# Performance work log

Measured on AMD Instinct MI355X. Metric: run time of the kernel, lower is better.

The kernel has to match this reference:

```python
import jax, jax.numpy as jnp
import numpy as np

N = 100000       # nodes
E = 1600000      # edges (avg degree 16)
F_IN = 128
F_OUT = 128
EPS = 1e-5       # GraphNorm eps
NEG_SLOPE = 0.01 # nn.LeakyReLU default


def setup_inputs() -> dict:
    key = jax.random.key(0)
    ks = jax.random.split(key, 4)
    x = jax.random.normal(ks[0], (N, F_IN), dtype=jnp.float32)
    edge_index = jax.random.randint(ks[1], (2, E), 0, N, dtype=jnp.int64)
    # GCNConv linear weight (stored as [in, out] for x @ W)
    W = jax.random.normal(ks[2], (F_IN, F_OUT), dtype=jnp.float32) / np.sqrt(F_IN).astype(np.float32)
    b = jnp.zeros((F_OUT,), jnp.float32)          # GCNConv bias
    gn_weight = jnp.ones((F_OUT,), jnp.float32)   # GraphNorm weight
    gn_bias = jnp.zeros((F_OUT,), jnp.float32)    # GraphNorm bias
    gn_mean_scale = jnp.ones((F_OUT,), jnp.float32)  # GraphNorm mean_scale
    return {"x": x, "edge_index": edge_index, "W": W, "b": b,
            "gn_weight": gn_weight, "gn_bias": gn_bias, "gn_mean_scale": gn_mean_scale}


def reference(x, edge_index, W, b, gn_weight, gn_bias, gn_mean_scale):
    n = x.shape[0]
    # --- GCNConv with add_self_loops=True, symmetric normalization ---
    loops = jnp.arange(n, dtype=edge_index.dtype)
    src = jnp.concatenate([edge_index[0], loops])  # [E+N]
    dst = jnp.concatenate([edge_index[1], loops])  # [E+N]
    deg = jax.ops.segment_sum(jnp.ones(src.shape, x.dtype), dst, num_segments=n)  # [N]
    deg_inv_sqrt = jnp.where(deg > 0, 1.0 / jnp.sqrt(deg), 0.0)
    norm = deg_inv_sqrt[src] * deg_inv_sqrt[dst]   # [E+N]
    h = x @ W                                      # [N, F_OUT]
    agg = jax.ops.segment_sum(h[src] * norm[:, None], dst, num_segments=n) + b  # [N, F_OUT]
    # --- GraphNorm (single graph: stats over all nodes, per-feature) ---
    mean = jnp.mean(agg, axis=0)                   # [F_OUT]
    centered = agg - mean * gn_mean_scale
    var = jnp.mean(centered * centered, axis=0)
    out = centered / jnp.sqrt(var + EPS) * gn_weight + gn_bias
    # --- LeakyReLU ---
    out = jnp.where(out > 0, out, NEG_SLOPE * out)
    return (out, edge_index)
```

## Files before the change

kernel.cpp:

```cpp
#include <hip/hip_runtime.h>

#define NN 100000
#define NE 1600000
#define F  128
#define NSPL 50000

#define SH   8
#define NPB  256
#define NBKT 391
#define B1   256
#define CH1  6250
#define MATN (NBKT * B1)
#define MATP (98 * 1024)
#define BCAP2 6144

#define SB   256

constexpr float EPS   = 1e-5f;
constexpr float SLOPE = 0.01f;

typedef __attribute__((ext_vector_type(8))) short short8;
typedef __attribute__((ext_vector_type(4))) float f32x4;
typedef __attribute__((ext_vector_type(2))) float f32x2;

__device__ inline unsigned int bf16rne(float f) {
    unsigned int u = __float_as_uint(f);
    return (u + 0x7fffu + ((u >> 16) & 1u)) >> 16;
}
__device__ inline float blo(unsigned int u) { return __uint_as_float(u << 16); }
__device__ inline float bhi(unsigned int u) { return __uint_as_float(u & 0xffff0000u); }
__device__ inline unsigned int pack2(float a, float b) {
    return bf16rne(a) | (bf16rne(b) << 16);
}
__device__ inline f32x2 pkadd(f32x2 a, f32x2 b) {
    f32x2 d;
    asm("v_pk_add_f32 %0, %1, %2" : "=v"(d) : "v"(a), "v"(b));
    return d;
}
__device__ inline f32x2 up2n(unsigned int u) {
    f32x2 r;
    r.x = __uint_as_float(u << 16);
    r.y = __uint_as_float(u);
    return r;
}

__global__ void k_wprep(const float* __restrict__ Wm, unsigned int* __restrict__ Wt) {
    int idx = blockIdx.x * 256 + threadIdx.x;
    int p = idx & 3, lane = (idx >> 2) & 63, n = (idx >> 8) & 7, kk = idx >> 11;
    int k0 = kk * 32 + (lane >> 4) * 8 + 2 * p;
    int c  = n * 16 + (lane & 15);
    unsigned int lo = bf16rne(Wm[k0 * F + c]);
    unsigned int hi = bf16rne(Wm[(k0 + 1) * F + c]);
    Wt[idx] = lo | (hi << 16);
}

__global__ __launch_bounds__(1024) void k_hist1(const int* __restrict__ dst,
                                                unsigned int* __restrict__ mat) {
    __shared__ unsigned int h[NBKT];
    if (threadIdx.x < NBKT) h[threadIdx.x] = 0u;
    __syncthreads();
    const int e0 = blockIdx.x * CH1;
    for (int i = threadIdx.x; i < CH1; i += 1024)
        atomicAdd(&h[dst[e0 + i] >> SH], 1u);
    __syncthreads();
    if (threadIdx.x < NBKT) mat[threadIdx.x * B1 + blockIdx.x] = h[threadIdx.x];
}

__global__ __launch_bounds__(1024) void k_scanA(const unsigned int* __restrict__ mat,
                                                unsigned int* __restrict__ scn,
                                                unsigned int* __restrict__ bsums) {
    __shared__ unsigned int ps[1024];
    const int t = threadIdx.x;
    const int i = blockIdx.x * 1024 + t;
    unsigned int v = mat[i];
    ps[t] = v;
    __syncthreads();
    for (int off = 1; off < 1024; off <<= 1) {
        unsigned int a = (t >= off) ? ps[t - off] : 0u;
        __syncthreads();
        ps[t] += a;
        __syncthreads();
    }
    scn[i] = ps[t];
    if (t == 1023) bsums[blockIdx.x] = ps[1023];
}

__global__ __launch_bounds__(128) void k_scanB(const unsigned int* __restrict__ bsums,
                                               unsigned int* __restrict__ boff) {
    __shared__ unsigned int ps[128];
    const int t = threadIdx.x;
    unsigned int v = (t < 98) ? bsums[t] : 0u;
    ps[t] = v;
    __syncthreads();
    for (int off = 1; off < 128; off <<= 1) {
        unsigned int a = (t >= off) ? ps[t - off] : 0u;
        __syncthreads();
        ps[t] += a;
        __syncthreads();
    }
    if (t < 98) boff[t] = ps[t] - v;
}


__global__ __launch_bounds__(1024) void k_scat1(const int* __restrict__ ei,
                                                const unsigned int* __restrict__ mat,
                                                const unsigned int* __restrict__ scn,
                                                const unsigned int* __restrict__ boff,
                                                unsigned int* __restrict__ ebuf) {
    __shared__ unsigned int cur[NBKT];
    if (threadIdx.x < NBKT) {
        int idx = threadIdx.x * B1 + blockIdx.x;
        cur[threadIdx.x] = scn[idx] + boff[idx >> 10] - mat[idx];
    }
    __syncthreads();
    const int e0 = blockIdx.x * CH1;
    for (int i = threadIdx.x; i < CH1; i += 1024) {
        int s = ei[e0 + i];
        int d = ei[NE + e0 + i];
        unsigned int pos = atomicAdd(&cur[d >> SH], 1u);
        ebuf[pos] = ((unsigned int)(d & (NPB - 1)) << 17) | (unsigned int)s;
    }
}

__global__ __launch_bounds__(256) void k_fill2(const unsigned int* __restrict__ mat,
                                               const unsigned int* __restrict__ scn,
                                               const unsigned int* __restrict__ boff,
                                               const unsigned int* __restrict__ ebuf,
                                               int* __restrict__ row_start,
                                               float* __restrict__ dis,
                                               int* __restrict__ csr) {
    __shared__ unsigned int stage[BCAP2];
    __shared__ unsigned int hist[NPB];
    __shared__ unsigned int cur[NPB];
    __shared__ unsigned int ps[NPB];
    const int t = threadIdx.x;
    const int bkt = blockIdx.x;
    hist[t] = 0u;
    __syncthreads();
    const int i0 = bkt * B1;
    const unsigned int ebase = scn[i0] + boff[i0 >> 10] - mat[i0];
    unsigned int eend;
    if (bkt == NBKT - 1) eend = (unsigned int)NE;
    else {
        const int i1 = (bkt + 1) * B1;
        eend = scn[i1] + boff[i1 >> 10] - mat[i1];
    }
    const unsigned int n = eend - ebase;
    const unsigned int m = (n < BCAP2) ? n : BCAP2;
    for (unsigned int i = t; i < m; i += 256) {
        unsigned int v = ebuf[ebase + i];
        stage[i] = v;
        atomicAdd(&hist[v >> 17], 1u);
    }
    for (unsigned int i = BCAP2 + t; i < n; i += 256)
        atomicAdd(&hist[ebuf[ebase + i] >> 17], 1u);
    __syncthreads();
    const unsigned int deg = hist[t];
    ps[t] = deg;
    __syncthreads();
    for (int off = 1; off < 256; off <<= 1) {
        unsigned int a = (t >= off) ? ps[t - off] : 0u;
        __syncthreads();
        ps[t] += a;
        __syncthreads();
    }
    const unsigned int ex = (t == 0) ? 0u : ps[t - 1];
    cur[t] = ebase + ex;
    const int node = bkt * NPB + t;
    if (node <= NN) row_start[node] = (int)(ebase + ex);
    if (node < NN)  dis[node] = rsqrtf((float)(deg + 1u));
    __syncthreads();
    for (unsigned int i = t; i < m; i += 256) {
        unsigned int v = stage[i];
        unsigned int pos = atomicAdd(&cur[v >> 17], 1u);
        csr[pos] = (int)(v & 0x1FFFFu);
    }
    for (unsigned int i = BCAP2 + t; i < n; i += 256) {
        unsigned int v = ebuf[ebase + i];
        unsigned int pos = atomicAdd(&cur[v >> 17], 1u);
        csr[pos] = (int)(v & 0x1FFFFu);
    }
}

__global__ __launch_bounds__(256) void k_gemm(const float* __restrict__ x,
                                              const unsigned int* __restrict__ Wt,
                                              const float* __restrict__ dis,
                                              unsigned short* __restrict__ g16) {
    __shared__ unsigned int xl[128 * 64];
    const int tid = threadIdx.x;
    const int lane = tid & 63, wave = tid >> 6;
    const int row0 = blockIdx.x * 128;

#pragma unroll
    for (int i = 0; i < 16; ++i) {
        int fi = i * 256 + tid;
        int lr = fi >> 5;
        int cf = (fi & 31) * 4;
        int gr = row0 + lr; if (gr >= NN) gr = NN - 1;
        float4 v = *(const float4*)(x + (size_t)gr * F + cf);
        unsigned int u0 = pack2(v.x, v.y);
        unsigned int u1 = pack2(v.z, v.w);
        int cu = (cf >> 1) ^ ((lr & 7) << 2);
        uint2 w2; w2.x = u0; w2.y = u1;
        *(uint2*)&xl[lr * 64 + cu] = w2;
    }
    __syncthreads();

    const int rbase = row0 + wave * 32;
    short8 afr[2][4];
#pragma unroll
    for (int m = 0; m < 2; ++m) {
        int lr = wave * 32 + m * 16 + (lane & 15);
#pragma unroll
        for (int kk = 0; kk < 4; ++kk) {
            int cu = (kk * 16 + (lane >> 4) * 4) ^ ((lr & 7) << 2);
            afr[m][kk] = *(const short8*)&xl[lr * 64 + cu];
        }
    }

    f32x4 acc[2][8];
#pragma unroll
    for (int m = 0; m < 2; ++m)
#pragma unroll
        for (int n = 0; n < 8; ++n) { f32x4 z = {0.f, 0.f, 0.f, 0.f}; acc[m][n] = z; }

    const uint4* Wt4 = (const uint4*)Wt;
#pragma unroll
    for (int kk = 0; kk < 4; ++kk) {
        union { uint4 u; short8 s; } bfr[8];
#pragma unroll
        for (int n = 0; n < 8; ++n) bfr[n].u = Wt4[(kk * 8 + n) * 64 + lane];
#pragma unroll
        for (int m = 0; m < 2; ++m)
#pragma unroll
            for (int n = 0; n < 8; ++n)
                acc[m][n] = __builtin_amdgcn_mfma_f32_16x16x32_bf16(afr[m][kk], bfr[n].s, acc[m][n], 0, 0, 0);
    }

    float dv[2][4];
#pragma unroll
    for (int m = 0; m < 2; ++m)
#pragma unroll
        for (int r = 0; r < 4; ++r) {
            int row = rbase + m * 16 + (lane >> 4) * 4 + r;
            dv[m][r] = (row < NN) ? dis[row] : 0.0f;
        }
#pragma unroll
    for (int m = 0; m < 2; ++m)
#pragma unroll
        for (int n = 0; n < 8; ++n)
#pragma unroll
            for (int r = 0; r < 4; ++r) {
                int row = rbase + m * 16 + (lane >> 4) * 4 + r;
                if (row < NN) {
                    int col = n * 16 + (lane & 15);
                    g16[(size_t)row * F + col] = (unsigned short)bf16rne(acc[m][n][r] * dv[m][r]);
                }
            }
}

__global__ __launch_bounds__(256) void k_gather(const unsigned int* __restrict__ g,
                                                const int* __restrict__ csr,
                                                const int* __restrict__ row_start,
                                                const float* __restrict__ dis,
                                                const float* __restrict__ b,
                                                unsigned int* __restrict__ agg_lo,
                                                unsigned int* __restrict__ agg_hi) {
    const int lane = threadIdx.x & 63;
    const int node = blockIdx.x * 4 + (threadIdx.x >> 6);
    if (node >= NN) return;
    const int q = lane >> 4;
    const int c = lane & 15;
    const int j = row_start[node];
    const int e = row_start[node + 1];
    const int L = e - j + 1;
    int sv = (j + lane < e) ? csr[j + lane] : node;
    f32x2 A0 = {0.f, 0.f}, A1 = A0, A2 = A0, A3 = A0;
    int k = 0;
    const int L1 = (L < 64) ? L : 64;
    for (; k < L1; k += 16) {
        int k0 = k + q, k1 = k0 + 4, k2 = k0 + 8, k3 = k0 + 12;
        int r0 = __shfl(sv, k0);
        int r1 = __shfl(sv, k1);
        int r2 = __shfl(sv, k2);
        int r3 = __shfl(sv, k3);
        bool p0 = k0 < L, p1 = k1 < L, p2 = k2 < L, p3 = k3 < L;
        uint4 v0, v1, v2, v3;
        if (p0) v0 = *(const uint4*)&g[(size_t)r0 * 64 + c * 4];
        if (p1) v1 = *(const uint4*)&g[(size_t)r1 * 64 + c * 4];
        if (p2) v2 = *(const uint4*)&g[(size_t)r2 * 64 + c * 4];
        if (p3) v3 = *(const uint4*)&g[(size_t)r3 * 64 + c * 4];
        if (p0) {
            A0 = pkadd(A0, up2n(v0.x)); A1 = pkadd(A1, up2n(v0.y));
            A2 = pkadd(A2, up2n(v0.z)); A3 = pkadd(A3, up2n(v0.w));
        }
        if (p1) {
            A0 = pkadd(A0, up2n(v1.x)); A1 = pkadd(A1, up2n(v1.y));
            A2 = pkadd(A2, up2n(v1.z)); A3 = pkadd(A3, up2n(v1.w));
        }
        if (p2) {
            A0 = pkadd(A0, up2n(v2.x)); A1 = pkadd(A1, up2n(v2.y));
            A2 = pkadd(A2, up2n(v2.z)); A3 = pkadd(A3, up2n(v2.w));
        }
        if (p3) {
            A0 = pkadd(A0, up2n(v3.x)); A1 = pkadd(A1, up2n(v3.y));
            A2 = pkadd(A2, up2n(v3.z)); A3 = pkadd(A3, up2n(v3.w));
        }
    }
    for (; k < L; k += 16) {
#pragma unroll
        for (int s = 0; s < 4; ++s) {
            int ks = k + q + s * 4;
            if (ks < L) {
                int rs = (j + ks < e) ? csr[j + ks] : node;
                uint4 v = *(const uint4*)&g[(size_t)rs * 64 + c * 4];
                A0 = pkadd(A0, up2n(v.x)); A1 = pkadd(A1, up2n(v.y));
                A2 = pkadd(A2, up2n(v.z)); A3 = pkadd(A3, up2n(v.w));
            }
        }
    }
#define RED2(A) A.x += __shfl_xor(A.x, 16); A.x += __shfl_xor(A.x, 32); \
                A.y += __shfl_xor(A.y, 16); A.y += __shfl_xor(A.y, 32);
    RED2(A0) RED2(A1) RED2(A2) RED2(A3)
#undef RED2
    if (q == 0) {
        float d = dis[node];
        const float4* bp = (const float4*)&b[c * 8];
        float4 b0 = bp[0], b1 = bp[1];
        uint4 w;
        w.x = pack2(b0.x + d * A0.x, b0.y + d * A0.y);
        w.y = pack2(b0.z + d * A1.x, b0.w + d * A1.y);
        w.z = pack2(b1.x + d * A2.x, b1.y + d * A2.y);
        w.w = pack2(b1.z + d * A3.x, b1.w + d * A3.y);
        unsigned int* base = (node < NSPL) ? (agg_lo + (size_t)node * 64)
                                           : (agg_hi + (size_t)(node - NSPL) * 64);
        *(uint4*)(base + c * 4) = w;
    }
}

__global__ __launch_bounds__(256) void k_stats(const unsigned int* __restrict__ agg_lo,
                                               const unsigned int* __restrict__ agg_hi,
                                               float* __restrict__ partials) {
    __shared__ float lds[4][16][16];
    const int tid = threadIdx.x;
    const int lane = tid & 63, wave = tid >> 6;
    const uint4* lo4 = (const uint4*)agg_lo;
    const uint4* hi4 = (const uint4*)agg_hi;
    const long totalLo = (long)NSPL * 16;
    const long total   = (long)NN * 16;
    const long stride  = (long)SB * 256;
    float s[8], qq[8];
#pragma unroll
    for (int i = 0; i < 8; ++i) { s[i] = 0.f; qq[i] = 0.f; }
    for (long i = (long)blockIdx.x * 256 + tid; i < total; i += stride) {
        uint4 v = (i < totalLo) ? lo4[i] : hi4[i - totalLo];
        float f0 = blo(v.x), f1 = bhi(v.x), f2 = blo(v.y), f3 = bhi(v.y);
        float f4 = blo(v.z), f5 = bhi(v.z), f6 = blo(v.w), f7 = bhi(v.w);
        s[0] += f0; qq[0] += f0 * f0;  s[1] += f1; qq[1] += f1 * f1;
        s[2] += f2; qq[2] += f2 * f2;  s[3] += f3; qq[3] += f3 * f3;
        s[4] += f4; qq[4] += f4 * f4;  s[5] += f5; qq[5] += f5 * f5;
        s[6] += f6; qq[6] += f6 * f6;  s[7] += f7; qq[7] += f7 * f7;
    }
#pragma unroll
    for (int i = 0; i < 8; ++i) {
        s[i]  += __shfl_xor(s[i], 16);  s[i]  += __shfl_xor(s[i], 32);
        qq[i] += __shfl_xor(qq[i], 16); qq[i] += __shfl_xor(qq[i], 32);
    }
    if (lane < 16) {
#pragma unroll
        for (int i = 0; i < 8; ++i) {
            lds[wave][lane][i]     = s[i];
            lds[wave][lane][i + 8] = qq[i];
        }
    }
    __syncthreads();
    const int c4n = tid >> 4, slot = tid & 15;
    float v = lds[0][c4n][slot] + lds[1][c4n][slot] + lds[2][c4n][slot] + lds[3][c4n][slot];
    int f = c4n * 8 + (slot & 7);
    int idx = (slot < 8) ? f : (F + f);
    partials[(size_t)blockIdx.x * 256 + idx] = v;
}

__global__ __launch_bounds__(256) void k_red(const float* __restrict__ partials,
                                             float* __restrict__ stats) {
    float a0 = 0.f, a1 = 0.f, a2 = 0.f, a3 = 0.f;
    for (int bq = 0; bq < SB; bq += 4) {
        a0 += partials[(bq + 0) * 256 + threadIdx.x];
        a1 += partials[(bq + 1) * 256 + threadIdx.x];
        a2 += partials[(bq + 2) * 256 + threadIdx.x];
        a3 += partials[(bq + 3) * 256 + threadIdx.x];
    }
    stats[threadIdx.x] = (a0 + a1) + (a2 + a3);
}

__global__ __launch_bounds__(256) void k_normei(const unsigned int* __restrict__ agg_lo,
                                               const unsigned int* __restrict__ agg_hi,
                                               const float* __restrict__ stats,
                                               const float* __restrict__ gw,
                                               const float* __restrict__ gb,
                                               const float* __restrict__ gms,
                                               float* __restrict__ out0,
                                               const int* __restrict__ ei,
                                               float* __restrict__ out1) {
    __shared__ float A[F], Bc[F];
    if (threadIdx.x < F) {
        int f = threadIdx.x;
        const float invn = 1.0f / (float)NN;
        float mean = stats[f] * invn;
        float ms = mean * gms[f];
        float var = stats[F + f] * invn - 2.0f * ms * mean + ms * ms;
        float inv = rsqrtf(var + EPS);
        float a = inv * gw[f];
        A[f] = a;
        Bc[f] = gb[f] - ms * a;
    }
    __syncthreads();
    const int c4 = threadIdx.x & 15;
    float ra[8], rb[8];
#pragma unroll
    for (int i = 0; i < 8; ++i) { ra[i] = A[c4 * 8 + i]; rb[i] = Bc[c4 * 8 + i]; }
    const uint4* lo4 = (const uint4*)agg_lo;
    const uint4* hi4 = (const uint4*)agg_hi;
    const int4* ei4 = (const int4*)ei;
    float4* o14 = (float4*)out1;
    const long totalLo = (long)NSPL * 16;
    const long total   = (long)NN * 16;
    const long stride  = (long)gridDim.x * 256;
    for (long i = (long)blockIdx.x * 256 + threadIdx.x; i < total; i += stride) {
        bool isLo = i < totalLo;
        uint4 v = isLo ? lo4[i] : hi4[i - totalLo];
        float f0 = blo(v.x) * ra[0] + rb[0], f1 = bhi(v.x) * ra[1] + rb[1];
        float f2 = blo(v.y) * ra[2] + rb[2], f3 = bhi(v.y) * ra[3] + rb[3];
        float f4 = blo(v.z) * ra[4] + rb[4], f5 = bhi(v.z) * ra[5] + rb[5];
        float f6 = blo(v.w) * ra[6] + rb[6], f7 = bhi(v.w) * ra[7] + rb[7];
        f0 = f0 > 0.f ? f0 : SLOPE * f0;  f1 = f1 > 0.f ? f1 : SLOPE * f1;
        f2 = f2 > 0.f ? f2 : SLOPE * f2;  f3 = f3 > 0.f ? f3 : SLOPE * f3;
        f4 = f4 > 0.f ? f4 : SLOPE * f4;  f5 = f5 > 0.f ? f5 : SLOPE * f5;
        f6 = f6 > 0.f ? f6 : SLOPE * f6;  f7 = f7 > 0.f ? f7 : SLOPE * f7;
        float4 r0, r1;
        r0.x = f0; r0.y = f1; r0.z = f2; r0.w = f3;
        r1.x = f4; r1.y = f5; r1.z = f6; r1.w = f7;
        float* op = out0 + i * 8;
        *(float4*)op = r0;
        *(float4*)(op + 4) = r1;
        if (isLo) {
            int4 ev = ei4[i];
            unsigned int z;
            asm("v_and_b32 %0, 0, %1" : "=v"(z) : "v"(v.x));
            float4 r;
            r.x = (float)(ev.x | (int)z);
            r.y = (float)ev.y;
            r.z = (float)ev.z;
            r.w = (float)ev.w;
            o14[i] = r;
        }
    }
}

extern "C" void kernel_launch(void* const* d_in, const int* in_sizes, int n_in,
                              void* d_out, int out_size, void* d_ws, size_t ws_size,
                              hipStream_t stream) {
    const float* x   = (const float*)d_in[0];
    const int*   ei  = (const int*)d_in[1];
    const float* Wm  = (const float*)d_in[2];
    const float* b   = (const float*)d_in[3];
    const float* gw  = (const float*)d_in[4];
    const float* gb  = (const float*)d_in[5];
    const float* gms = (const float*)d_in[6];

    float* out  = (float*)d_out;
    float* out1 = out + (size_t)NN * F;
    unsigned int* agg_lo = (unsigned int*)out1;

    unsigned int* wsu   = (unsigned int*)d_ws;
    unsigned int* g     = wsu;
    unsigned int* ebuf  = wsu;
    unsigned int* mat   = g + (size_t)NN * 64;
    unsigned int* scn   = mat + MATP;
    unsigned int* bsums = scn + MATP;
    unsigned int* boff  = bsums + 128;
    int* row_start      = (int*)(boff + 128);
    int* csr            = row_start + NN + 2;
    float* dis          = (float*)(csr + NE + 8);
    float* stats        = dis + NN;
    unsigned int* Wt    = (unsigned int*)(stats + 256);
    unsigned int* agg_hi = Wt + 8192;
    float* partials     = (float*)(agg_hi + (size_t)(NN - NSPL) * 64);

    k_wprep<<<32, 256, 0, stream>>>(Wm, Wt);
    k_hist1<<<B1, 1024, 0, stream>>>(ei + NE, mat);
    k_scanA<<<98, 1024, 0, stream>>>(mat, scn, bsums);
    k_scanB<<<1, 128, 0, stream>>>(bsums, boff);
    k_scat1<<<B1, 1024, 0, stream>>>(ei, mat, scn, boff, ebuf);
    k_fill2<<<NBKT, 256, 0, stream>>>(mat, scn, boff, ebuf, row_start, dis, csr);
    k_gemm<<<(NN + 127) / 128, 256, 0, stream>>>(x, Wt, dis, (unsigned short*)g);
    k_gather<<<NN / 4, 256, 0, stream>>>(g, csr, row_start, dis, b, agg_lo, agg_hi);
    k_stats<<<SB, 256, 0, stream>>>(agg_lo, agg_hi, partials);
    k_red<<<1, 256, 0, stream>>>(partials, stats);
    k_normei<<<1024, 256, 0, stream>>>(agg_lo, agg_hi, stats, gw, gb, gms, out, ei, out1);
}
```

Before: 164.6 us.

## Fold weight prep and block-offset scan into neighbours, vectorize GEMM stores

Weight bf16 packing moves into the histogram kernel, and the single-block offset scan is recomputed redundantly inside the scatter and fill kernels, removing two kernel launches. The GEMM swaps MFMA operand order so each lane holds four consecutive output columns, allowing packed 8-byte bf16 stores instead of scalar 2-byte stores. The normalization launch grid is also doubled. The trade-off is redundant scan work per block and extra barriers in the scatter and fill kernels.

```diff
diff --git a/kernel.cpp b/kernel.cpp
--- a/kernel.cpp
+++ b/kernel.cpp
@@ -44,21 +44,22 @@
     return r;
 }
 
-__global__ void k_wprep(const float* __restrict__ Wm, unsigned int* __restrict__ Wt) {
-    int idx = blockIdx.x * 256 + threadIdx.x;
-    int p = idx & 3, lane = (idx >> 2) & 63, n = (idx >> 8) & 7, kk = idx >> 11;
-    int k0 = kk * 32 + (lane >> 4) * 8 + 2 * p;
-    int c  = n * 16 + (lane & 15);
-    unsigned int lo = bf16rne(Wm[k0 * F + c]);
-    unsigned int hi = bf16rne(Wm[(k0 + 1) * F + c]);
-    Wt[idx] = lo | (hi << 16);
-}
-
 __global__ __launch_bounds__(1024) void k_hist1(const int* __restrict__ dst,
-                                                unsigned int* __restrict__ mat) {
+                                                unsigned int* __restrict__ mat,
+                                                const float* __restrict__ Wm,
+                                                unsigned int* __restrict__ Wt) {
     __shared__ unsigned int h[NBKT];
     if (threadIdx.x < NBKT) h[threadIdx.x] = 0u;
     __syncthreads();
+    if (blockIdx.x < 8) {
+        int idx = blockIdx.x * 1024 + threadIdx.x;
+        int p = idx & 3, lane = (idx >> 2) & 63, n = (idx >> 8) & 7, kk = idx >> 11;
+        int k0 = kk * 32 + (lane >> 4) * 8 + 2 * p;
+        int c  = n * 16 + (lane & 15);
+        unsigned int lo = bf16rne(Wm[k0 * F + c]);
+        unsigned int hi = bf16rne(Wm[(k0 + 1) * F + c]);
+        Wt[idx] = lo | (hi << 16);
+    }
     const int e0 = blockIdx.x * CH1;
     for (int i = threadIdx.x; i < CH1; i += 1024)
         atomicAdd(&h[dst[e0 + i] >> SH], 1u);
@@ -85,36 +86,36 @@
     if (t == 1023) bsums[blockIdx.x] = ps[1023];
 }
 
-__global__ __launch_bounds__(128) void k_scanB(const unsigned int* __restrict__ bsums,
-                                               unsigned int* __restrict__ boff) {
-    __shared__ unsigned int ps[128];
-    const int t = threadIdx.x;
-    unsigned int v = (t < 98) ? bsums[t] : 0u;
-    ps[t] = v;
-    __syncthreads();
-    for (int off = 1; off < 128; off <<= 1) {
-        unsigned int a = (t >= off) ? ps[t - off] : 0u;
-        __syncthreads();
-        ps[t] += a;
-        __syncthreads();
-    }
-    if (t < 98) boff[t] = ps[t] - v;
-}
-
 
 __global__ __launch_bounds__(1024) void k_scat1(const int* __restrict__ ei,
                                                 const unsigned int* __restrict__ mat,
                                                 const unsigned int* __restrict__ scn,
-                                                const unsigned int* __restrict__ boff,
+                                                const unsigned int* __restrict__ bsums,
                                                 unsigned int* __restrict__ ebuf) {
     __shared__ unsigned int cur[NBKT];
-    if (threadIdx.x < NBKT) {
-        int idx = threadIdx.x * B1 + blockIdx.x;
-        cur[threadIdx.x] = scn[idx] + boff[idx >> 10] - mat[idx];
+    __shared__ unsigned int bo[128];
+    const int t = threadIdx.x;
+    if (t < 128) {
+        unsigned int v = (t < 98) ? bsums[t] : 0u;
+        bo[t] = v;
+        for (int off = 1; off < 128; off <<= 1) {
+            __syncthreads();
+            unsigned int a = (t >= off) ? bo[t - off] : 0u;
+            __syncthreads();
+            bo[t] += a;
+        }
+        bo[t] -= v;
+    } else {
+        for (int off = 1; off < 128; off <<= 1) { __syncthreads(); __syncthreads(); }
+    }
+    __syncthreads();
+    if (t < NBKT) {
+        int idx = t * B1 + blockIdx.x;
+        cur[t] = scn[idx] + bo[idx >> 10] - mat[idx];
     }
     __syncthreads();
     const int e0 = blockIdx.x * CH1;
-    for (int i = threadIdx.x; i < CH1; i += 1024) {
+    for (int i = t; i < CH1; i += 1024) {
         int s = ei[e0 + i];
         int d = ei[NE + e0 + i];
         unsigned int pos = atomicAdd(&cur[d >> SH], 1u);
@@ -124,7 +125,7 @@
 
 __global__ __launch_bounds__(256) void k_fill2(const unsigned int* __restrict__ mat,
                                                const unsigned int* __restrict__ scn,
-                                               const unsigned int* __restrict__ boff,
+                                               const unsigned int* __restrict__ bsums,
                                                const unsigned int* __restrict__ ebuf,
                                                int* __restrict__ row_start,
                                                float* __restrict__ dis,
@@ -133,17 +134,31 @@
     __shared__ unsigned int hist[NPB];
     __shared__ unsigned int cur[NPB];
     __shared__ unsigned int ps[NPB];
+    __shared__ unsigned int bo[128];
     const int t = threadIdx.x;
     const int bkt = blockIdx.x;
     hist[t] = 0u;
+    if (t < 128) {
+        unsigned int v = (t < 98) ? bsums[t] : 0u;
+        bo[t] = v;
+        for (int off = 1; off < 128; off <<= 1) {
+            __syncthreads();
+            unsigned int a = (t >= off) ? bo[t - off] : 0u;
+            __syncthreads();
+            bo[t] += a;
+        }
+        bo[t] -= v;
+    } else {
+        for (int off = 1; off < 128; off <<= 1) { __syncthreads(); __syncthreads(); }
+    }
     __syncthreads();
     const int i0 = bkt * B1;
-    const unsigned int ebase = scn[i0] + boff[i0 >> 10] - mat[i0];
+    const unsigned int ebase = scn[i0] + bo[i0 >> 10] - mat[i0];
     unsigned int eend;
     if (bkt == NBKT - 1) eend = (unsigned int)NE;
     else {
         const int i1 = (bkt + 1) * B1;
-        eend = scn[i1] + boff[i1 >> 10] - mat[i1];
+        eend = scn[i1] + bo[i1 >> 10] - mat[i1];
     }
     const unsigned int n = eend - ebase;
     const unsigned int m = (n < BCAP2) ? n : BCAP2;
@@ -234,29 +249,23 @@
         for (int m = 0; m < 2; ++m)
 #pragma unroll
             for (int n = 0; n < 8; ++n)
-                acc[m][n] = __builtin_amdgcn_mfma_f32_16x16x32_bf16(afr[m][kk], bfr[n].s, acc[m][n], 0, 0, 0);
-    }
-
-    float dv[2][4];
-#pragma unroll
-    for (int m = 0; m < 2; ++m)
-#pragma unroll
-        for (int r = 0; r < 4; ++r) {
-            int row = rbase + m * 16 + (lane >> 4) * 4 + r;
-            dv[m][r] = (row < NN) ? dis[row] : 0.0f;
-        }
-#pragma unroll
-    for (int m = 0; m < 2; ++m)
-#pragma unroll
-        for (int n = 0; n < 8; ++n)
-#pragma unroll
-            for (int r = 0; r < 4; ++r) {
-                int row = rbase + m * 16 + (lane >> 4) * 4 + r;
-                if (row < NN) {
-                    int col = n * 16 + (lane & 15);
-                    g16[(size_t)row * F + col] = (unsigned short)bf16rne(acc[m][n][r] * dv[m][r]);
-                }
-            }
+                acc[m][n] = __builtin_amdgcn_mfma_f32_16x16x32_bf16(bfr[n].s, afr[m][kk], acc[m][n], 0, 0, 0);
+    }
+
+#pragma unroll
+    for (int m = 0; m < 2; ++m) {
+        int xr = rbase + m * 16 + (lane & 15);
+        bool ok = xr < NN;
+        float d = ok ? dis[xr] : 0.0f;
+        unsigned short* gp = g16 + (size_t)(ok ? xr : 0) * F + (lane >> 4) * 4;
+#pragma unroll
+        for (int n = 0; n < 8; ++n) {
+            uint2 w;
+            w.x = pack2(acc[m][n][0] * d, acc[m][n][1] * d);
+            w.y = pack2(acc[m][n][2] * d, acc[m][n][3] * d);
+            if (ok) *(uint2*)(gp + n * 16) = w;
+        }
+    }
 }
 
 __global__ __launch_bounds__(256) void k_gather(const unsigned int* __restrict__ g,
@@ -478,8 +487,7 @@
     unsigned int* mat   = g + (size_t)NN * 64;
     unsigned int* scn   = mat + MATP;
     unsigned int* bsums = scn + MATP;
-    unsigned int* boff  = bsums + 128;
-    int* row_start      = (int*)(boff + 128);
+    int* row_start      = (int*)(bsums + 128);
     int* csr            = row_start + NN + 2;
     float* dis          = (float*)(csr + NE + 8);
     float* stats        = dis + NN;
@@ -487,15 +495,13 @@
     unsigned int* agg_hi = Wt + 8192;
     float* partials     = (float*)(agg_hi + (size_t)(NN - NSPL) * 64);
 
-    k_wprep<<<32, 256, 0, stream>>>(Wm, Wt);
-    k_hist1<<<B1, 1024, 0, stream>>>(ei + NE, mat);
+    k_hist1<<<B1, 1024, 0, stream>>>(ei + NE, mat, Wm, Wt);
     k_scanA<<<98, 1024, 0, stream>>>(mat, scn, bsums);
-    k_scanB<<<1, 128, 0, stream>>>(bsums, boff);
-    k_scat1<<<B1, 1024, 0, stream>>>(ei, mat, scn, boff, ebuf);
-    k_fill2<<<NBKT, 256, 0, stream>>>(mat, scn, boff, ebuf, row_start, dis, csr);
+    k_scat1<<<B1, 1024, 0, stream>>>(ei, mat, scn, bsums, ebuf);
+    k_fill2<<<NBKT, 256, 0, stream>>>(mat, scn, bsums, ebuf, row_start, dis, csr);
     k_gemm<<<(NN + 127) / 128, 256, 0, stream>>>(x, Wt, dis, (unsigned short*)g);
     k_gather<<<NN / 4, 256, 0, stream>>>(g, csr, row_start, dis, b, agg_lo, agg_hi);
     k_stats<<<SB, 256, 0, stream>>>(agg_lo, agg_hi, partials);
     k_red<<<1, 256, 0, stream>>>(partials, stats);
-    k_normei<<<1024, 256, 0, stream>>>(agg_lo, agg_hi, stats, gw, gb, gms, out, ei, out1);
-}
+    k_normei<<<2048, 256, 0, stream>>>(agg_lo, agg_hi, stats, gw, gb, gms, out, ei, out1);
+}
```

New measurement: 155.8 us. 1.06x faster.
